# Performance work log

Hardware: AMD Instinct MI355X
Metric: run time of the kernel (lower is better)

The kernel has to match this reference:

```python
import jax, jax.numpy as jnp
import numpy as np

# Hyperparameters matching init_kwargs / repo defaults
MARGIN = 0.2
ALPHA = 0.1          # opt.alpha
OT_ITER = 20         # opt.OT_iteration
BETA = 0.5           # IPOT temperature (hardcoded in repo's OT module)
SIM_TYPE = "MISA"    # opt.sim_type_dot
MAX_VIOLATION = True
EPS = 1e-12

N_IMAGE = 128
N_REG = 36
D = 1024
MAX_WORD = 60


def _matchmap_sim(M):
    # M: (n_image, n_regions, n_word)
    if SIM_TYPE == "SISA":
        return M.mean(axis=2).mean(axis=1)
    elif SIM_TYPE == "MISA":
        return M.max(axis=1).mean(axis=1)
    elif SIM_TYPE == "SIMA":
        return M.max(axis=2).mean(axis=1)
    raise ValueError


def _ipot_distance(C, n, m):
    # C: (bs, n, m) cosine-distance cost; IPOT with uniform marginals.
    bs = C.shape[0]
    # Torch code detaches T, so no gradient flows through the iteration.
    A = jnp.exp(-jax.lax.stop_gradient(C) / BETA)

    def body(_, carry):
        T, sigma = carry
        Q = A * T                                            # (bs, n, m)
        delta = 1.0 / (n * jnp.matmul(Q, sigma))             # (bs, n, 1)
        sigma = 1.0 / (m * jnp.matmul(Q.transpose(0, 2, 1), delta))  # (bs, m, 1)
        T = delta * Q * sigma.transpose(0, 2, 1)
        return (T, sigma)

    T0 = jnp.ones((bs, n, m), C.dtype)
    s0 = jnp.ones((bs, m, 1), C.dtype) / m
    T, _ = jax.lax.fori_loop(0, OT_ITER, body, (T0, s0))
    T = jax.lax.stop_gradient(T)
    # batch_trace(C^T T) == sum(C * T) per batch element
    return -jnp.sum(C * T, axis=(1, 2))                      # (bs,)


def _scores(im, s, cap_lens):
    n_reg = im.shape[1]
    imn = im / (jnp.linalg.norm(im, axis=2, keepdims=True) + EPS)
    lens = np.asarray(cap_lens)
    sims, sims_ot = [], []
    for i in range(s.shape[0]):  # ragged per-caption loop (as in original)
        n_word = int(lens[i])
        cap = s[i, :n_word, :]                               # (w, d)
        # matchmap: bmm(images, cap^T) -> (n_image, n_regions, n_word)
        M = jnp.einsum('brd,wd->brw', im, cap)
        sims.append(_matchmap_sim(M))
        capn = cap / (jnp.linalg.norm(cap, axis=1, keepdims=True) + EPS)
        # cost_matrix_batch_torch(cap^T, img^T).transpose -> (n_image, n_reg, n_word)
        C = 1.0 - jnp.einsum('brd,wd->brw', imn, capn)
        sims_ot.append(_ipot_distance(C, n_reg, n_word))
    return jnp.stack(sims, axis=1), jnp.stack(sims_ot, axis=1)  # (n_img, n_cap)


def _loss(im, s, cap_lens):
    scores, scores_ot = _scores(im, s, cap_lens)
    n = scores.shape[0]
    eye = jnp.eye(n, dtype=bool)

    def costs(sc):
        d = jnp.diag(sc)[:, None]                            # (n, 1)
        cs = jnp.clip(MARGIN + sc - d, 0.0)                  # caption-side
        ci = jnp.clip(MARGIN + sc - d.T, 0.0)                # image-side
        cs = jnp.where(eye, 0.0, cs)
        ci = jnp.where(eye, 0.0, ci)
        return cs, ci

    cost_s, cost_im = costs(scores)
    cost_s_ot, cost_im_ot = costs(scores_ot)
    cost_s = cost_s + ALPHA * cost_s_ot
    cost_im = cost_im + ALPHA * cost_im_ot
    if MAX_VIOLATION:
        cost_s = cost_s.max(axis=1)
        cost_im = cost_im.max(axis=0)
        cost_s_ot = cost_s_ot.max(axis=1)
        cost_im_ot = cost_im_ot.max(axis=0)
    return (cost_s.sum() + cost_im.sum(), cost_s_ot.sum() + cost_im_ot.sum())


def setup_inputs() -> dict:
    key = jax.random.key(0)
    k1, k2, k3 = jax.random.split(key, 3)
    im = jax.random.normal(k1, (N_IMAGE, N_REG, D), dtype=jnp.float32)
    s = jax.random.normal(k2, (N_IMAGE, MAX_WORD, D), dtype=jnp.float32)
    rng = np.random.default_rng(0)
    s_l = np.asarray(rng.integers(10, MAX_WORD + 1, size=N_IMAGE), dtype=np.int64)
    x = jax.random.normal(k3, (1,), dtype=jnp.float32)  # unused by forward math
    return {"im": im, "s": s, "s_l": s_l, "x": x}


def reference(im, s, s_l, x):
    return _loss(im, s, s_l)
```

## Files before the change

kernel.cpp:

```cpp
#include <hip/hip_runtime.h>
#include <hip/hip_bf16.h>
#include <math.h>

#define N_IMAGE 128
#define N_REG   36
#define DIM     1024
#define MAX_WORD 60
#define OT_ITERS 20
#define MARGIN_F 0.2f
#define ALPHA_F  0.1f
#define EPS_F    1e-12f

#define APAN  16384
#define AIMG  (3 * APAN)
#define BCAP  (4 * APAN)

typedef short bf16x8 __attribute__((ext_vector_type(8)));
typedef float f32x4  __attribute__((ext_vector_type(4)));
typedef float f32x2  __attribute__((ext_vector_type(2)));


__device__ __forceinline__ unsigned int pkbf2(float a, float b) {
    union { __hip_bfloat162 h2; unsigned int u; } cv;
    cv.h2 = __float22bfloat162_rn(make_float2(a, b));
    return cv.u;
}
__device__ __forceinline__ float lo16(unsigned int u) { return __int_as_float((int)(u << 16)); }
__device__ __forceinline__ float hi16(unsigned int u) { return __int_as_float((int)(u & 0xFFFF0000u)); }

#define SWZ(x, pat) __int_as_float(__builtin_amdgcn_ds_swizzle(__float_as_int(x), (pat)))
#define BPERM(a, x) __int_as_float(__builtin_amdgcn_ds_bpermute((a), __float_as_int(x)))
#define DPPADD(x, ctrl) \
    ((x) + __int_as_float(__builtin_amdgcn_update_dpp(0, __float_as_int(x), (ctrl), 0xf, 0xf, true)))

__device__ __forceinline__ float bfly16_sum(float x) {
    x = DPPADD(x, 0xB1);
    x = DPPADD(x, 0x4E);
    x = DPPADD(x, 0x124);
    x = DPPADD(x, 0x128);
    return x;
}

__device__ __forceinline__ float xq_sum(float x) {
    x += SWZ(x, 0x401F);
    const int xaddr = (((int)(threadIdx.x & 63) ^ 32) << 2);
    x += BPERM(xaddr, x);
    return x;
}
__device__ __forceinline__ float xq_max(float x) {
    x = fmaxf(x, SWZ(x, 0x401F));
    const int xaddr = (((int)(threadIdx.x & 63) ^ 32) << 2);
    x = fmaxf(x, BPERM(xaddr, x));
    return x;
}
__device__ __forceinline__ float bfly64_sum(float x) {
    return xq_sum(bfly16_sum(x));
}


__global__ __launch_bounds__(256) void pack_kernel(
    const float* __restrict__ im, const float* __restrict__ s,
    float* __restrict__ inv_im, float* __restrict__ inv_cap,
    float* __restrict__ out,
    unsigned short* __restrict__ imp, unsigned short* __restrict__ sp,
    const int* __restrict__ s_l, int* __restrict__ perm) {

    const int pid = blockIdx.x;
    const int tid = threadIdx.x;

    if (pid == 896) {
        if (tid < N_IMAGE) {
            const int mt = s_l[tid];
            int rank = 0;
            for (int j = 0; j < N_IMAGE; ++j) {
                const int mj = s_l[j];
                rank += (mj > mt) || (mj == mt && j < tid);
            }
            perm[rank] = tid;
        }
        return;
    }
    if (pid == 0 && tid == 0) { out[0] = 0.0f; out[1] = 0.0f; }

    const int w = tid >> 6, lane = tid & 63, q = lane >> 4, l15 = lane & 15;
    const bool isim = (pid < 384);
    int obj, p, nvalid;
    const float* src;
    unsigned short* dst;
    if (isim) {
        obj = pid / 3; p = pid % 3;
        src = im + (size_t)obj * 36 * DIM;
        dst = imp + (size_t)obj * AIMG + (size_t)p * APAN;
        nvalid = 36;
    } else {
        const int k = pid - 384;
        obj = k >> 2; p = k & 3;
        src = s + (size_t)obj * 60 * DIM;
        dst = sp + (size_t)obj * BCAP + (size_t)p * APAN;
        nvalid = 60;
    }
    const int row = p * 16 + l15;
    const bool valid = (row < nvalid);

    float ss = 0.0f;
    #pragma unroll
    for (int i = 0; i < 4; ++i) {
        const int c = w * 4 + i;
        #pragma unroll
        for (int h = 0; h < 2; ++h) {
            float4 v0 = make_float4(0.f, 0.f, 0.f, 0.f), v1 = v0;
            if (valid) {
                const float* rp = src + (size_t)row * DIM + c * 64 + h * 32 + q * 8;
                v0 = *(const float4*)rp;
                v1 = *(const float4*)(rp + 4);
            }
            ss += v0.x * v0.x + v0.y * v0.y + v0.z * v0.z + v0.w * v0.w
                + v1.x * v1.x + v1.y * v1.y + v1.z * v1.z + v1.w * v1.w;
            uint4 o;
            o.x = pkbf2(v0.x, v0.y); o.y = pkbf2(v0.z, v0.w);
            o.z = pkbf2(v1.x, v1.y); o.w = pkbf2(v1.z, v1.w);
            *(uint4*)(dst + (size_t)c * 1024 + h * 512 + q * 128 + l15 * 8) = o;
        }
    }
    ss = xq_sum(ss);
    __shared__ float sh[4][16];
    if (lane < 16) sh[w][lane] = ss;
    __syncthreads();
    if (tid < 16) {
        const float t = sh[0][tid] + sh[1][tid] + sh[2][tid] + sh[3][tid];
        const int r = p * 16 + tid;
        if (r < nvalid) {
            const float inv = 1.0f / (sqrtf(t) + EPS_F);
            if (isim) inv_im[obj * 36 + r] = inv;
            else      inv_cap[obj * 60 + r] = inv;
        }
    }
}


__global__ void norms_kernel(const float* __restrict__ im, const float* __restrict__ s,
                             float* __restrict__ inv_im, float* __restrict__ inv_cap,
                             float* __restrict__ out) {
    if (blockIdx.x == 0 && threadIdx.x == 0) { out[0] = 0.0f; out[1] = 0.0f; }
    const int NIM = N_IMAGE * N_REG;
    const int NS  = N_IMAGE * MAX_WORD;
    int row  = blockIdx.x * 4 + (threadIdx.x >> 6);
    int lane = threadIdx.x & 63;
    if (row >= NIM + NS) return;
    const bool isim = (row < NIM);
    const float* base = isim ? (im + (size_t)row * DIM)
                             : (s  + (size_t)(row - NIM) * DIM);
    const float4* b4 = (const float4*)base;
    float acc = 0.0f;
    for (int k = lane; k < DIM / 4; k += 64) {
        float4 v = b4[k];
        acc += v.x * v.x + v.y * v.y + v.z * v.z + v.w * v.w;
    }
    for (int off = 32; off; off >>= 1) acc += __shfl_down(acc, off, 64);
    if (lane == 0) {
        float inv = 1.0f / (sqrtf(acc) + EPS_F);
        if (isim) inv_im[row] = inv;
        else      inv_cap[row - NIM] = inv;
    }
}


template <int CT>
__device__ __forceinline__ void build_apk(
    f32x4 (&acc)[3 * CT], const float* invImS, const float* invCapS,
    int m, int wv, int q, int l15,
    unsigned int (*apk)[(CT + 1) / 2], float* mxv, bool* vw) {

    constexpr int PK = (CT + 1) / 2;
    float icap2[CT];
    #pragma unroll
    for (int ct = 0; ct < CT; ++ct) {
        const int w = ct * 16 + l15;
        vw[ct]    = (w < m);
        icap2[ct] = (w < 60) ? 2.0f * invCapS[w] : 0.0f;
    }
    #pragma unroll
    for (int ct = 0; ct < CT; ++ct) mxv[ct] = -3e38f;

    #pragma unroll
    for (int j = 0; j < 12; ++j) {
        const int rt = j >> 2, p = j & 3;
        const int r  = rt * 16 + q * 4 + p;
        const bool rowok = (rt < 2) || (q == 0);
        const float iir = rowok ? invImS[wv * 36 + (r < 36 ? r : 0)] : 0.0f;
        float av[CT];
        #pragma unroll
        for (int ct = 0; ct < CT; ++ct) {
            const float Mv = acc[rt * CT + ct][p];
            mxv[ct] = fmaxf(mxv[ct], rowok ? Mv : -3e38f);
            const bool ok = rowok && vw[ct];
            av[ct] = ok ? __expf(fmaf(Mv, iir * icap2[ct], -2.0f)) : 0.0f;
        }
        #pragma unroll
        for (int pk = 0; pk < PK; ++pk)
            apk[j][pk] = pkbf2(av[2 * pk], (2 * pk + 1 < CT) ? av[2 * pk + 1] : 0.0f);
    }

    {
        const int baddr = l15 << 2;
        #pragma unroll
        for (int pk = 0; pk < PK; ++pk) {
            const int r0 = __builtin_amdgcn_ds_bpermute(baddr, (int)apk[8][pk]);
            const int r1 = __builtin_amdgcn_ds_bpermute(baddr, (int)apk[9][pk]);
            const int r2 = __builtin_amdgcn_ds_bpermute(baddr, (int)apk[10][pk]);
            const int r3 = __builtin_amdgcn_ds_bpermute(baddr, (int)apk[11][pk]);
            const int lo = (q & 1) ? r1 : r0;
            const int hi = (q & 1) ? r3 : r2;
            apk[8][pk] = (unsigned int)((q & 2) ? hi : lo);
        }
    }
}


template <int CT>
__device__ __forceinline__ float ot_iterate(
    f32x2 (*af)[(CT + 1) / 2], const bool* vw, float mf, float inv_m) {

    constexpr int PK = (CT + 1) / 2;
    f32x2 t2[9][PK];
    f32x2 sig2[PK];
    #pragma unroll
    for (int pk = 0; pk < PK; ++pk) {
        const bool v0 = vw[2 * pk];
        const bool v1 = (2 * pk + 1 < CT) && vw[2 * pk + 1];
        sig2[pk].x = v0 ? inv_m : 0.0f;
        sig2[pk].y = v1 ? inv_m : 0.0f;
        #pragma unroll
        for (int j = 0; j < 9; ++j) {
            t2[j][pk].x = v0 ? mf : 0.0f;
            t2[j][pk].y = v1 ? mf : 0.0f;
        }
    }

    for (int it = 0; it < OT_ITERS; ++it) {
        f32x2 s2[PK], csum[PK];
        #pragma unroll
        for (int pk = 0; pk < PK; ++pk) {
            s2[pk]   = sig2[pk] * sig2[pk];
            csum[pk] = (f32x2){0.0f, 0.0f};
        }
        #pragma unroll
        for (int j = 0; j < 9; ++j) {
            f32x2 at[PK];
            #pragma unroll
            for (int pk = 0; pk < PK; ++pk)
                at[pk] = af[j][pk] * t2[j][pk];
            f32x2 u2 = at[0] * s2[0];
            #pragma unroll
            for (int pk = 1; pk < PK; ++pk) u2 += at[pk] * s2[pk];
            const float R  = bfly16_sum(u2.x + u2.y);
            const float dl = __builtin_amdgcn_rcpf(36.0f * R);
            f32x2 dl2; dl2.x = dl; dl2.y = dl;
            #pragma unroll
            for (int pk = 0; pk < PK; ++pk) {
                const f32x2 tn = at[pk] * (dl2 * sig2[pk]);
                t2[j][pk] = tn;
                csum[pk] += tn;
            }
        }
        #pragma unroll
        for (int pk = 0; pk < PK; ++pk) {
            const float cx = xq_sum(csum[pk].x);
            const float cy = xq_sum(csum[pk].y);
            const bool v0 = vw[2 * pk];
            const bool v1 = (2 * pk + 1 < CT) && vw[2 * pk + 1];
            sig2[pk].x = v0 ? __builtin_amdgcn_rcpf(mf * cx) : 0.0f;
            sig2[pk].y = v1 ? __builtin_amdgcn_rcpf(mf * cy) : 0.0f;
        }
    }

    float pp = 0.0f;
    #pragma unroll
    for (int j = 0; j < 9; ++j) {
        #pragma unroll
        for (int pk = 0; pk < PK; ++pk) {
            const float cvx = -0.5f * __logf(fmaxf(af[j][pk].x, 1e-30f));
            pp = fmaf(cvx, t2[j][pk].x * sig2[pk].x, pp);
            if (2 * pk + 1 < CT) {
                const float cvy = -0.5f * __logf(fmaxf(af[j][pk].y, 1e-30f));
                pp = fmaf(cvy, t2[j][pk].y * sig2[pk].y, pp);
            }
        }
    }
    return bfly64_sum(pp);
}


template <int CT>
__device__ __forceinline__ void misa_write(
    const float* mxv, const bool* vw, float inv_m, int lane,
    float* __restrict__ S, int b, int cap) {
    float sp = 0.0f;
    #pragma unroll
    for (int ct = 0; ct < CT; ++ct) {
        float v = xq_max(mxv[ct]);
        sp += vw[ct] ? v : 0.0f;
    }
    sp = bfly64_sum(sp);
    if (lane == 0) S[(size_t)b * N_IMAGE + cap] = sp * inv_m * 0.25f;
}


template <int CT>
__device__ __forceinline__ void gemm_core(
    const unsigned short* __restrict__ imp, const unsigned short* __restrict__ sp,
    int cap, int b0, int wv, int q, int l15, f32x4 (&acc)[3 * CT]) {

    const unsigned short* Ab = imp + (size_t)(b0 + wv) * AIMG + (q * 128 + l15 * 8);
    const unsigned short* Bb = sp  + (size_t)cap * BCAP        + (q * 128 + l15 * 8);

    #pragma unroll
    for (int t = 0; t < 3 * CT; ++t) acc[t] = (f32x4){0.f, 0.f, 0.f, 0.f};

    bf16x8 a0[3], bf0[CT], a1[3], bf1[CT];
    #pragma unroll
    for (int rt = 0; rt < 3; ++rt) a0[rt] = *(const bf16x8*)(Ab + rt * APAN);
    #pragma unroll
    for (int ct = 0; ct < CT; ++ct) bf0[ct] = *(const bf16x8*)(Bb + ct * APAN);

    #pragma unroll 1
    for (int c = 0; c < 16; ++c) {
        const unsigned short* Ac = Ab + c * 1024;
        const unsigned short* Bc = Bb + c * 1024;
        #pragma unroll
        for (int rt = 0; rt < 3; ++rt) a1[rt] = *(const bf16x8*)(Ac + rt * APAN + 512);
        #pragma unroll
        for (int ct = 0; ct < CT; ++ct) bf1[ct] = *(const bf16x8*)(Bc + ct * APAN + 512);
        #pragma unroll
        for (int rt = 0; rt < 3; ++rt)
            #pragma unroll
            for (int ct = 0; ct < CT; ++ct)
                acc[rt * CT + ct] = __builtin_amdgcn_mfma_f32_16x16x32_bf16(
                    a0[rt], bf0[ct], acc[rt * CT + ct], 0, 0, 0);
        const int cn = (c < 15) ? c + 1 : 15;
        const unsigned short* An = Ab + cn * 1024;
        const unsigned short* Bn = Bb + cn * 1024;
        #pragma unroll
        for (int rt = 0; rt < 3; ++rt) a0[rt] = *(const bf16x8*)(An + rt * APAN);
        #pragma unroll
        for (int ct = 0; ct < CT; ++ct) bf0[ct] = *(const bf16x8*)(Bn + ct * APAN);
        #pragma unroll
        for (int rt = 0; rt < 3; ++rt)
            #pragma unroll
            for (int ct = 0; ct < CT; ++ct)
                acc[rt * CT + ct] = __builtin_amdgcn_mfma_f32_16x16x32_bf16(
                    a1[rt], bf1[ct], acc[rt * CT + ct], 0, 0, 0);
    }
}


template <int CT>
__device__ __forceinline__ void pair_body_fast(
    const unsigned short* __restrict__ imp, const unsigned short* __restrict__ sp,
    const float* invImS, const float* invCapS,
    int cap, int b0, int m,
    float* __restrict__ S, float* __restrict__ SOT) {

    const int tid  = threadIdx.x;
    const int lane = tid & 63;
    const int wv   = tid >> 6;
    const int q    = lane >> 4;
    const int l15  = lane & 15;
    const float mf    = (float)m;
    const float inv_m = 1.0f / mf;
    constexpr int PK = (CT + 1) / 2;

    f32x4 acc[3 * CT];
    gemm_core<CT>(imp, sp, cap, b0, wv, q, l15, acc);

    __syncthreads();

    unsigned int apk[12][PK];
    float mxv[CT]; bool vw[CT];
    build_apk<CT>(acc, invImS, invCapS, m, wv, q, l15, apk, mxv, vw);

    f32x2 af[9][PK];
    #pragma unroll
    for (int j = 0; j < 9; ++j)
        #pragma unroll
        for (int pk = 0; pk < PK; ++pk) {
            af[j][pk].x = lo16(apk[j][pk]);
            af[j][pk].y = hi16(apk[j][pk]);
        }

    const int b = b0 + wv;
    misa_write<CT>(mxv, vw, inv_m, lane, S, b, cap);
    const float pp = ot_iterate<CT>(af, vw, mf, inv_m);
    if (lane == 0) SOT[(size_t)b * N_IMAGE + cap] = -pp;
}

__global__ __launch_bounds__(256, 4)
void pair_fast(const unsigned short* __restrict__ imp,
               const unsigned short* __restrict__ sp,
               const int* __restrict__ s_l,
               const int* __restrict__ perm,
               const float* __restrict__ inv_im, const float* __restrict__ inv_cap,
               float* __restrict__ S, float* __restrict__ SOT) {
    const int bid = blockIdx.x;
    const int cap = perm[bid >> 5];
    const int b0  = (bid & 31) * 4;
    const int tid = threadIdx.x;

    __shared__ float invImS[144];
    __shared__ float invCapS[60];
    if (tid < 144) invImS[tid] = inv_im[b0 * 36 + tid];
    else if (tid < 204) invCapS[tid - 144] = inv_cap[cap * 60 + (tid - 144)];

    const int m  = s_l[cap];
    const int CT = __builtin_amdgcn_readfirstlane((m + 15) >> 4);
    switch (CT) {
    case 1: pair_body_fast<1>(imp, sp, invImS, invCapS, cap, b0, m, S, SOT); break;
    case 2: pair_body_fast<2>(imp, sp, invImS, invCapS, cap, b0, m, S, SOT); break;
    case 3: pair_body_fast<3>(imp, sp, invImS, invCapS, cap, b0, m, S, SOT); break;
    default: pair_body_fast<4>(imp, sp, invImS, invCapS, cap, b0, m, S, SOT); break;
    }
}


template <int CT>
__device__ __forceinline__ void pair_body_slow(
    const float* __restrict__ im, const float* __restrict__ s,
    char* smem, const float* invImS, const float* invCapS,
    int cap, int b0, int m,
    float* __restrict__ S, float* __restrict__ SOT) {

    const int tid  = threadIdx.x;
    const int lane = tid & 63;
    const int wv   = tid >> 6;
    const int q    = lane >> 4;
    const int l15  = lane & 15;
    const int q4   = tid & 15;
    const int row0 = tid >> 4;
    const float mf    = (float)m;
    const float inv_m = 1.0f / mf;
    constexpr int PK = (CT + 1) / 2;

    const char* sA = smem;
    const char* sB = smem + 27648;

    f32x4 acc[3 * CT];
    #pragma unroll
    for (int t = 0; t < 3 * CT; ++t) acc[t] = (f32x4){0.f, 0.f, 0.f, 0.f};

    for (int c = 0; c < 16; ++c) {
        const int col = c * 64 + q4 * 4;
        #pragma unroll
        for (int img = 0; img < 4; ++img) {
            #pragma unroll
            for (int j = 0; j < 3; ++j) {
                const int r = row0 + 16 * j;
                if (j < 2 || row0 < 4) {
                    const size_t ro = (size_t)(b0 * 36 + img * 36 + r) * 1024 + col;
                    float4 v = *(const float4*)(im + ro);
                    uint2 w2; w2.x = pkbf2(v.x, v.y); w2.y = pkbf2(v.z, v.w);
                    *(uint2*)(smem + (img * 48 + r) * 144 + q4 * 8) = w2;
                }
            }
        }
        #pragma unroll
        for (int j = 0; j < CT; ++j) {
            const int r = row0 + 16 * j;
            if (CT < 4 || j < 3 || row0 < 12) {
                const size_t ro = (size_t)(cap * 60 + r) * 1024 + col;
                float4 v = *(const float4*)(s + ro);
                uint2 w2; w2.x = pkbf2(v.x, v.y); w2.y = pkbf2(v.z, v.w);
                *(uint2*)(smem + (192 + r) * 144 + q4 * 8) = w2;
            }
        }
        __syncthreads();
        #pragma unroll
        for (int h = 0; h < 2; ++h) {
            bf16x8 bfr[CT];
            #pragma unroll
            for (int ct = 0; ct < CT; ++ct)
                bfr[ct] = *(const bf16x8*)(sB + (ct * 16 + l15) * 144 + h * 64 + q * 16);
            #pragma unroll
            for (int rt = 0; rt < 3; ++rt) {
                bf16x8 afr = *(const bf16x8*)(sA + (wv * 48 + rt * 16 + l15) * 144 + h * 64 + q * 16);
                #pragma unroll
                for (int ct = 0; ct < CT; ++ct)
                    acc[rt * CT + ct] = __builtin_amdgcn_mfma_f32_16x16x32_bf16(
                        afr, bfr[ct], acc[rt * CT + ct], 0, 0, 0);
            }
        }
        __syncthreads();
    }

    unsigned int apk[12][PK];
    float mxv[CT]; bool vw[CT];
    build_apk<CT>(acc, invImS, invCapS, m, wv, q, l15, apk, mxv, vw);

    f32x2 af[9][PK];
    #pragma unroll
    for (int j = 0; j < 9; ++j)
        #pragma unroll
        for (int pk = 0; pk < PK; ++pk) {
            af[j][pk].x = lo16(apk[j][pk]);
            af[j][pk].y = hi16(apk[j][pk]);
        }

    const int b = b0 + wv;
    misa_write<CT>(mxv, vw, inv_m, lane, S, b, cap);
    const float pp = ot_iterate<CT>(af, vw, mf, inv_m);
    if (lane == 0) SOT[(size_t)b * N_IMAGE + cap] = -pp;
}

__global__ __launch_bounds__(256, 4)
void pair_slow(const float* __restrict__ im, const float* __restrict__ s,
               const int* __restrict__ s_l,
               const float* __restrict__ inv_im, const float* __restrict__ inv_cap,
               float* __restrict__ S, float* __restrict__ SOT) {
    const int cap = blockIdx.x;
    const int b0  = blockIdx.y * 4;
    const int tid = threadIdx.x;

    __shared__ __align__(16) char smem[36864];
    __shared__ float invImS[144];
    __shared__ float invCapS[60];

    if (tid < 144) invImS[tid] = inv_im[b0 * 36 + tid];
    else if (tid < 204) invCapS[tid - 144] = inv_cap[cap * 60 + (tid - 144)];

    const int m = s_l[cap];
    {
        float4 z = make_float4(0.f, 0.f, 0.f, 0.f);
        #pragma unroll
        for (int j = 0; j < 9; ++j)
            *(float4*)(smem + (tid + j * 256) * 16) = z;
    }
    __syncthreads();

    const int CT = __builtin_amdgcn_readfirstlane((m + 15) >> 4);
    switch (CT) {
    case 1: pair_body_slow<1>(im, s, smem, invImS, invCapS, cap, b0, m, S, SOT); break;
    case 2: pair_body_slow<2>(im, s, smem, invImS, invCapS, cap, b0, m, S, SOT); break;
    case 3: pair_body_slow<3>(im, s, smem, invImS, invCapS, cap, b0, m, S, SOT); break;
    default: pair_body_slow<4>(im, s, smem, invImS, invCapS, cap, b0, m, S, SOT); break;
    }
}


__global__ void loss_kernel(const float* __restrict__ S, const float* __restrict__ SOT,
                            float* __restrict__ out) {
    const int j = blockIdx.x;
    const int t = threadIdx.x;
    __shared__ float sh[4][2];
    const float db  = S[j * 129];
    const float dob = SOT[j * 129];
    float rv = 0.f, rov = 0.f, cv = 0.f, cov = 0.f;
    if (t != j) {
        float cs  = fmaxf(0.0f, MARGIN_F + S[j * 128 + t] - db);
        float cso = fmaxf(0.0f, MARGIN_F + SOT[j * 128 + t] - dob);
        rv = cs + ALPHA_F * cso;  rov = cso;
        float ci  = fmaxf(0.0f, MARGIN_F + S[t * 128 + j] - db);
        float cio = fmaxf(0.0f, MARGIN_F + SOT[t * 128 + j] - dob);
        cv = ci + ALPHA_F * cio;  cov = cio;
    }
    for (int off = 32; off; off >>= 1) {
        rv  = fmaxf(rv,  __shfl_down(rv,  off, 64));
        rov = fmaxf(rov, __shfl_down(rov, off, 64));
        cv  = fmaxf(cv,  __shfl_down(cv,  off, 64));
        cov = fmaxf(cov, __shfl_down(cov, off, 64));
    }
    if ((t & 63) == 0) {
        sh[0][t >> 6] = rv; sh[1][t >> 6] = rov;
        sh[2][t >> 6] = cv; sh[3][t >> 6] = cov;
    }
    __syncthreads();
    if (t == 0) {
        float a0 = fmaxf(sh[0][0], sh[0][1]) + fmaxf(sh[2][0], sh[2][1]);
        float a1 = fmaxf(sh[1][0], sh[1][1]) + fmaxf(sh[3][0], sh[3][1]);
        atomicAdd(&out[0], a0);
        atomicAdd(&out[1], a1);
    }
}

extern "C" void kernel_launch(void* const* d_in, const int* in_sizes, int n_in,
                              void* d_out, int out_size, void* d_ws, size_t ws_size,
                              hipStream_t stream) {
    const float* im  = (const float*)d_in[0];
    const float* s   = (const float*)d_in[1];
    const int*   s_l = (const int*)d_in[2];
    float* out = (float*)d_out;
    float* ws  = (float*)d_ws;

    float* inv_im  = ws;
    float* inv_cap = ws + 4608;
    float* S       = ws + 12288;
    float* SOT     = ws + 28672;
    int*   perm    = (int*)(ws + 45056);
    unsigned short* imp = (unsigned short*)((char*)d_ws + 180736);
    unsigned short* sp  = imp + (size_t)N_IMAGE * AIMG;
    const size_t need_fast = 180736 +
        ((size_t)N_IMAGE * AIMG + (size_t)N_IMAGE * BCAP) * 2;

    if (ws_size >= need_fast) {
        pack_kernel<<<dim3(897), dim3(256), 0, stream>>>(
            im, s, inv_im, inv_cap, out, imp, sp, s_l, perm);
        pair_fast<<<dim3(N_IMAGE * N_IMAGE / 4), dim3(256), 0, stream>>>(
            imp, sp, s_l, perm, inv_im, inv_cap, S, SOT);
    } else {
        norms_kernel<<<dim3((4608 + 7680) / 4), dim3(256), 0, stream>>>(
            im, s, inv_im, inv_cap, out);
        pair_slow<<<dim3(N_IMAGE, N_IMAGE / 4), dim3(256), 0, stream>>>(
            im, s, s_l, inv_im, inv_cap, S, SOT);
    }
    loss_kernel<<<dim3(N_IMAGE), dim3(128), 0, stream>>>(S, SOT, out);
}
```

Baseline: 257.9 us.

## Process two image groups per block for short captions with dual OT iteration

For captions with at most 32 words, each block now handles 8 images (two per wave) instead of 4. The two independent IPOT iterations are interleaved in one wave to raise instruction-level parallelism and hide shuffle latency, and the B fragments are loaded once and reused for both images. The pack kernel now counts long captions so blocks can be split between the single and dual paths, which halves the block count for the short-caption group. The cost is higher register pressure, which may reduce occupancy, and fewer blocks in flight for that group.

```diff
diff --git a/kernel.cpp b/kernel.cpp
--- a/kernel.cpp
+++ b/kernel.cpp
@@ -77,6 +77,11 @@
                 rank += (mj > mt) || (mj == mt && j < tid);
             }
             perm[rank] = tid;
+        }
+        if (tid == 0) {
+            int k = 0;
+            for (int j = 0; j < N_IMAGE; ++j) k += (s_l[j] > 32);
+            perm[128] = k;
         }
         return;
     }
@@ -167,8 +172,8 @@
 
 template <int CT>
 __device__ __forceinline__ void build_apk(
-    f32x4 (&acc)[3 * CT], const float* invImS, const float* invCapS,
-    int m, int wv, int q, int l15,
+    f32x4 (&acc)[3 * CT], const float* invImRow, const float* invCapS,
+    int m, int q, int l15,
     unsigned int (*apk)[(CT + 1) / 2], float* mxv, bool* vw) {
 
     constexpr int PK = (CT + 1) / 2;
@@ -187,7 +192,7 @@
         const int rt = j >> 2, p = j & 3;
         const int r  = rt * 16 + q * 4 + p;
         const bool rowok = (rt < 2) || (q == 0);
-        const float iir = rowok ? invImS[wv * 36 + (r < 36 ? r : 0)] : 0.0f;
+        const float iir = rowok ? invImRow[r < 36 ? r : 0] : 0.0f;
         float av[CT];
         #pragma unroll
         for (int ct = 0; ct < CT; ++ct) {
@@ -292,6 +297,71 @@
 
 
 template <int CT>
+__device__ __forceinline__ void ot_iterate_dual(
+    const f32x2* afa, const f32x2* afb, const bool* vw, float mf, float inv_m,
+    float& ppa, float& ppb) {
+
+    f32x2 ta[9], tb[9], siga, sigb;
+    const bool v0 = vw[0];
+    const bool v1 = (CT > 1) ? vw[1] : false;
+    siga.x = v0 ? inv_m : 0.0f; siga.y = v1 ? inv_m : 0.0f;
+    sigb = siga;
+    #pragma unroll
+    for (int j = 0; j < 9; ++j) {
+        ta[j].x = v0 ? mf : 0.0f; ta[j].y = v1 ? mf : 0.0f;
+        tb[j] = ta[j];
+    }
+
+    for (int it = 0; it < OT_ITERS; ++it) {
+        f32x2 s2a = siga * siga, s2b = sigb * sigb;
+        f32x2 csa = (f32x2){0.0f, 0.0f}, csb = (f32x2){0.0f, 0.0f};
+        #pragma unroll
+        for (int j = 0; j < 9; ++j) {
+            const f32x2 ata = afa[j] * ta[j];
+            const f32x2 atb = afb[j] * tb[j];
+            const f32x2 ua = ata * s2a;
+            const f32x2 ub = atb * s2b;
+            const float Ra = bfly16_sum(ua.x + ua.y);
+            const float Rb = bfly16_sum(ub.x + ub.y);
+            const float dla = __builtin_amdgcn_rcpf(36.0f * Ra);
+            const float dlb = __builtin_amdgcn_rcpf(36.0f * Rb);
+            f32x2 da; da.x = dla; da.y = dla;
+            f32x2 db; db.x = dlb; db.y = dlb;
+            const f32x2 tna = ata * (da * siga);
+            const f32x2 tnb = atb * (db * sigb);
+            ta[j] = tna; csa += tna;
+            tb[j] = tnb; csb += tnb;
+        }
+        const float cax = xq_sum(csa.x);
+        const float cay = xq_sum(csa.y);
+        const float cbx = xq_sum(csb.x);
+        const float cby = xq_sum(csb.y);
+        siga.x = v0 ? __builtin_amdgcn_rcpf(mf * cax) : 0.0f;
+        siga.y = v1 ? __builtin_amdgcn_rcpf(mf * cay) : 0.0f;
+        sigb.x = v0 ? __builtin_amdgcn_rcpf(mf * cbx) : 0.0f;
+        sigb.y = v1 ? __builtin_amdgcn_rcpf(mf * cby) : 0.0f;
+    }
+
+    float pa = 0.0f, pb = 0.0f;
+    #pragma unroll
+    for (int j = 0; j < 9; ++j) {
+        const float cax = -0.5f * __logf(fmaxf(afa[j].x, 1e-30f));
+        pa = fmaf(cax, ta[j].x * siga.x, pa);
+        const float cbx = -0.5f * __logf(fmaxf(afb[j].x, 1e-30f));
+        pb = fmaf(cbx, tb[j].x * sigb.x, pb);
+        if (CT > 1) {
+            const float cay = -0.5f * __logf(fmaxf(afa[j].y, 1e-30f));
+            pa = fmaf(cay, ta[j].y * siga.y, pa);
+            const float cby = -0.5f * __logf(fmaxf(afb[j].y, 1e-30f));
+            pb = fmaf(cby, tb[j].y * sigb.y, pb);
+        }
+    }
+    ppa = bfly64_sum(pa);
+    ppb = bfly64_sum(pb);
+}
+
+
+template <int CT>
 __device__ __forceinline__ void misa_write(
     const float* mxv, const bool* vw, float inv_m, int lane,
     float* __restrict__ S, int b, int cap) {
@@ -377,7 +447,7 @@
 
     unsigned int apk[12][PK];
     float mxv[CT]; bool vw[CT];
-    build_apk<CT>(acc, invImS, invCapS, m, wv, q, l15, apk, mxv, vw);
+    build_apk<CT>(acc, invImS + wv * 36, invCapS, m, q, l15, apk, mxv, vw);
 
     f32x2 af[9][PK];
     #pragma unroll
@@ -392,6 +462,85 @@
     misa_write<CT>(mxv, vw, inv_m, lane, S, b, cap);
     const float pp = ot_iterate<CT>(af, vw, mf, inv_m);
     if (lane == 0) SOT[(size_t)b * N_IMAGE + cap] = -pp;
+}
+
+
+template <int CT>
+__device__ __forceinline__ void pair_body_dual(
+    const unsigned short* __restrict__ imp, const unsigned short* __restrict__ sp,
+    const float* invImS , const float* invCapS,
+    int cap, int b0, int m,
+    float* __restrict__ S, float* __restrict__ SOT) {
+
+    const int tid  = threadIdx.x;
+    const int lane = tid & 63;
+    const int wv   = tid >> 6;
+    const int q    = lane >> 4;
+    const int l15  = lane & 15;
+    const float mf    = (float)m;
+    const float inv_m = 1.0f / mf;
+
+    const int off = q * 128 + l15 * 8;
+    const unsigned short* Aa  = imp + (size_t)(b0 + wv)     * AIMG + off;
+    const unsigned short* Ab2 = imp + (size_t)(b0 + 4 + wv) * AIMG + off;
+    const unsigned short* Bb  = sp  + (size_t)cap * BCAP + off;
+
+    f32x4 acca[3 * CT], accb[3 * CT];
+    #pragma unroll
+    for (int t = 0; t < 3 * CT; ++t) {
+        acca[t] = (f32x4){0.f, 0.f, 0.f, 0.f};
+        accb[t] = (f32x4){0.f, 0.f, 0.f, 0.f};
+    }
+
+    #pragma unroll 1
+    for (int c = 0; c < 16; ++c) {
+        #pragma unroll
+        for (int h = 0; h < 2; ++h) {
+            const int o = c * 1024 + h * 512;
+            bf16x8 bfr[CT], fa[3], fb[3];
+            #pragma unroll
+            for (int ct = 0; ct < CT; ++ct) bfr[ct] = *(const bf16x8*)(Bb + o + ct * APAN);
+            #pragma unroll
+            for (int rt = 0; rt < 3; ++rt) {
+                fa[rt] = *(const bf16x8*)(Aa  + o + rt * APAN);
+                fb[rt] = *(const bf16x8*)(Ab2 + o + rt * APAN);
+            }
+            #pragma unroll
+            for (int rt = 0; rt < 3; ++rt)
+                #pragma unroll
+                for (int ct = 0; ct < CT; ++ct) {
+                    acca[rt * CT + ct] = __builtin_amdgcn_mfma_f32_16x16x32_bf16(
+                        fa[rt], bfr[ct], acca[rt * CT + ct], 0, 0, 0);
+                    accb[rt * CT + ct] = __builtin_amdgcn_mfma_f32_16x16x32_bf16(
+                        fb[rt], bfr[ct], accb[rt * CT + ct], 0, 0, 0);
+                }
+        }
+    }
+
+    __syncthreads();
+
+    unsigned int apka[12][1], apkb[12][1];
+    float mxa[CT], mxb[CT]; bool vw[CT];
+    build_apk<CT>(acca, invImS + wv * 36,       invCapS, m, q, l15, apka, mxa, vw);
+    build_apk<CT>(accb, invImS + (4 + wv) * 36, invCapS, m, q, l15, apkb, mxb, vw);
+
+    f32x2 afa[9], afb[9];
+    #pragma unroll
+    for (int j = 0; j < 9; ++j) {
+        afa[j].x = lo16(apka[j][0]); afa[j].y = hi16(apka[j][0]);
+        afb[j].x = lo16(apkb[j][0]); afb[j].y = hi16(apkb[j][0]);
+    }
+
+    const int ba = b0 + wv, bb = b0 + 4 + wv;
+    misa_write<CT>(mxa, vw, inv_m, lane, S, ba, cap);
+    misa_write<CT>(mxb, vw, inv_m, lane, S, bb, cap);
+
+    float ppa, ppb;
+    ot_iterate_dual<CT>(afa, afb, vw, mf, inv_m, ppa, ppb);
+    if (lane == 0) {
+        SOT[(size_t)ba * N_IMAGE + cap] = -ppa;
+        SOT[(size_t)bb * N_IMAGE + cap] = -ppb;
+    }
 }
 
 __global__ __launch_bounds__(256, 4)
@@ -401,23 +550,32 @@
                const int* __restrict__ perm,
                const float* __restrict__ inv_im, const float* __restrict__ inv_cap,
                float* __restrict__ S, float* __restrict__ SOT) {
+    const int K   = perm[128];
     const int bid = blockIdx.x;
-    const int cap = perm[bid >> 5];
-    const int b0  = (bid & 31) * 4;
+    int cap, b0; bool dual;
+    if (bid < K * 32) {
+        cap = perm[bid >> 5]; b0 = (bid & 31) * 4; dual = false;
+    } else {
+        const int i = bid - K * 32;
+        if (i >= (N_IMAGE - K) * 16) return;
+        cap = perm[K + (i >> 4)]; b0 = (i & 15) * 8; dual = true;
+    }
     const int tid = threadIdx.x;
 
-    __shared__ float invImS[144];
+    __shared__ float invImS[288];
     __shared__ float invCapS[60];
-    if (tid < 144) invImS[tid] = inv_im[b0 * 36 + tid];
-    else if (tid < 204) invCapS[tid - 144] = inv_cap[cap * 60 + (tid - 144)];
+    const int nim = dual ? 288 : 144;
+    for (int t = tid; t < nim; t += 256) invImS[t] = inv_im[b0 * 36 + t];
+    if (tid >= 192 && tid < 252) invCapS[tid - 192] = inv_cap[cap * 60 + (tid - 192)];
 
     const int m  = s_l[cap];
     const int CT = __builtin_amdgcn_readfirstlane((m + 15) >> 4);
-    switch (CT) {
-    case 1: pair_body_fast<1>(imp, sp, invImS, invCapS, cap, b0, m, S, SOT); break;
-    case 2: pair_body_fast<2>(imp, sp, invImS, invCapS, cap, b0, m, S, SOT); break;
-    case 3: pair_body_fast<3>(imp, sp, invImS, invCapS, cap, b0, m, S, SOT); break;
-    default: pair_body_fast<4>(imp, sp, invImS, invCapS, cap, b0, m, S, SOT); break;
+    if (dual) {
+        if (CT == 1) pair_body_dual<1>(imp, sp, invImS, invCapS, cap, b0, m, S, SOT);
+        else         pair_body_dual<2>(imp, sp, invImS, invCapS, cap, b0, m, S, SOT);
+    } else {
+        if (CT == 3) pair_body_fast<3>(imp, sp, invImS, invCapS, cap, b0, m, S, SOT);
+        else         pair_body_fast<4>(imp, sp, invImS, invCapS, cap, b0, m, S, SOT);
     }
 }
 
@@ -493,7 +651,7 @@
 
     unsigned int apk[12][PK];
     float mxv[CT]; bool vw[CT];
-    build_apk<CT>(acc, invImS, invCapS, m, wv, q, l15, apk, mxv, vw);
+    build_apk<CT>(acc, invImS + wv * 36, invCapS, m, q, l15, apk, mxv, vw);
 
     f32x2 af[9][PK];
     #pragma unroll
@@ -594,9 +752,9 @@
     float* S       = ws + 12288;
     float* SOT     = ws + 28672;
     int*   perm    = (int*)(ws + 45056);
-    unsigned short* imp = (unsigned short*)((char*)d_ws + 180736);
+    unsigned short* imp = (unsigned short*)((char*)d_ws + 181248);
     unsigned short* sp  = imp + (size_t)N_IMAGE * AIMG;
-    const size_t need_fast = 180736 +
+    const size_t need_fast = 181248 +
         ((size_t)N_IMAGE * AIMG + (size_t)N_IMAGE * BCAP) * 2;
 
     if (ws_size >= need_fast) {
```

New measurement: 261.3 us. No clear change (+1.3%).
